# Kernel optimization log

Hardware: AMD Instinct MI355X
Metric: run time of the kernel (lower is better)

Reference implementation:

```python
import jax, jax.numpy as jnp
import numpy as np

N1, E1 = 102400, 300000
N2, E2 = 10240, 40960
N3, E3 = 1024, 4096
G = 64
D = 256   # node_dim == hidden_dim (forced by where(M==0, x, M))
B = 64    # bond_dim
DEPTHS = (3, 3, 4)


def _make_edges(rng, n_nodes, n_edges):
    # build mirrored directed edges so every edge has an exact reverse
    half = n_edges // 2
    u = rng.integers(0, n_nodes, half)
    v = rng.integers(0, n_nodes, half)
    src = np.concatenate([u, v])
    dst = np.concatenate([v, u])
    rev = np.concatenate([np.arange(half, n_edges), np.arange(0, half)])
    return np.stack([src, dst]).astype(np.int64), rev.astype(np.int64)


def _linear_params(key, fan_in, fan_out):
    k1, k2 = jax.random.split(key)
    s = 1.0 / np.sqrt(fan_in)
    W = jax.random.uniform(k1, (fan_in, fan_out), jnp.float32, -s, s)
    b = jax.random.uniform(k2, (fan_out,), jnp.float32, -s, s)
    return W, b


def setup_inputs() -> dict:
    rng = np.random.default_rng(0)
    key = jax.random.key(0)
    ks = jax.random.split(key, 16)

    ei1, rev1 = _make_edges(rng, N1, E1)
    ei2, rev2 = _make_edges(rng, N2, E2)
    ei3, rev3 = _make_edges(rng, N3, E3)

    inp = {
        "x": jax.random.normal(ks[0], (N1, D), jnp.float32),
        "edge_attr1": jax.random.normal(ks[1], (E1, B), jnp.float32),
        "edge_attr2": jax.random.normal(ks[2], (E2, B), jnp.float32),
        "edge_attr3": jax.random.normal(ks[3], (E3, B), jnp.float32),
        "edge_index1": jnp.asarray(ei1), "rev_edge_index1": jnp.asarray(rev1),
        "edge_index2": jnp.asarray(ei2), "rev_edge_index2": jnp.asarray(rev2),
        "edge_index3": jnp.asarray(ei3), "rev_edge_index3": jnp.asarray(rev3),
        "batch1_2": jnp.asarray(np.repeat(np.arange(N2), N1 // N2)),
        "batch2": jnp.asarray(np.repeat(np.arange(N3), N2 // N3)),
        "batch3": jnp.asarray(np.repeat(np.arange(G), N3 // G)),
    }
    kidx = 4
    for lvl in (1, 2, 3):
        Wi, bi = _linear_params(ks[kidx], D + B, D); kidx += 1
        Wh, bh = _linear_params(ks[kidx], D, D); kidx += 1
        Wo, bo = _linear_params(ks[kidx], D + D, D); kidx += 1
        inp[f"Wi{lvl}"], inp[f"bi{lvl}"] = Wi, bi
        inp[f"Wh{lvl}"], inp[f"bh{lvl}"] = Wh, bh
        inp[f"Wo{lvl}"], inp[f"bo{lvl}"] = Wo, bo
    return inp


def _bmp(x, src, dst, rev, ea, Wi, bi, Wh, bh, Wo, bo, depth):
    # BondMessagePassing.forward (dropout is identity in eval)
    n = x.shape[0]
    H0 = jax.nn.relu(jnp.concatenate([x[src], ea], axis=1) @ Wi + bi)  # [E, D]
    H = H0
    for _ in range(depth - 1):
        agg = jax.ops.segment_sum(H, dst, num_segments=n)              # [N, D]
        M = agg[src] - H[rev]
        H = jax.nn.relu(H0 + M @ Wh + bh)
    M = jax.ops.segment_sum(H, dst, num_segments=n)
    M = jnp.where(jnp.sum(M, axis=1, keepdims=True) == 0, x, M)
    return jax.nn.relu(jnp.concatenate([x, M], axis=1) @ Wo + bo)


def _mean_pool(h, seg, n):
    s = jax.ops.segment_sum(h, seg, num_segments=n)
    c = jax.ops.segment_sum(jnp.ones((h.shape[0], 1), h.dtype), seg, num_segments=n)
    return s / jnp.maximum(c, 1.0)


def reference(x, edge_attr1, edge_attr2, edge_attr3,
              edge_index1, rev_edge_index1, edge_index2, rev_edge_index2,
              edge_index3, rev_edge_index3, batch1_2, batch2, batch3,
              Wi1, bi1, Wh1, bh1, Wo1, bo1,
              Wi2, bi2, Wh2, bh2, Wo2, bo2,
              Wi3, bi3, Wh3, bh3, Wo3, bo3):
    h1 = _bmp(x, edge_index1[0], edge_index1[1], rev_edge_index1, edge_attr1,
              Wi1, bi1, Wh1, bh1, Wo1, bo1, DEPTHS[0])
    x2 = _mean_pool(h1, batch1_2, N2)
    h2 = _bmp(x2, edge_index2[0], edge_index2[1], rev_edge_index2, edge_attr2,
              Wi2, bi2, Wh2, bh2, Wo2, bo2, DEPTHS[1])
    x3 = _mean_pool(h2, batch2, N3)
    h3 = _bmp(x3, edge_index3[0], edge_index3[1], rev_edge_index3, edge_attr3,
              Wi3, bi3, Wh3, bh3, Wo3, bo3, DEPTHS[2])
    out = _mean_pool(h3, batch3, G)  # [G, D] subgraph3_pooled
    return out
```

## Files before the change

kernel.cpp:

```cpp
#include <hip/hip_runtime.h>
#include <stdint.h>

typedef __bf16 bf16;
typedef __bf16 bf16x4 __attribute__((ext_vector_type(4)));
typedef __bf16 bf16x8 __attribute__((ext_vector_type(8)));
typedef float  f32x4  __attribute__((ext_vector_type(4)));

__device__ __forceinline__ int clampi(int v, int n) { return (v < 0 || v >= n) ? 0 : v; }

__device__ __forceinline__ void gload16(const void* g, void* l) {
  __builtin_amdgcn_global_load_lds((const __attribute__((address_space(1))) void*)g,
                                   (__attribute__((address_space(3))) void*)l, 16, 0, 0);
}

__global__ void wtcvt_kernel(const float* __restrict__ W, bf16* __restrict__ Wt, int K) {
  int idx = blockIdx.x * 256 + threadIdx.x;
  if (idx >= K * 256) return;
  int k = idx >> 8, n = idx & 255;
  Wt[(size_t)n * K + k] = (bf16)W[idx];
}

__global__ void hist_kernel(const int* __restrict__ dst, int E, int* __restrict__ cnt, int N) {
  int e = blockIdx.x * 256 + threadIdx.x;
  if (e < E) atomicAdd(&cnt[clampi(dst[e], N)], 1);
}

__global__ void scan_block_kernel(const int* __restrict__ cnt, int N,
                                  int* __restrict__ incl, int* __restrict__ bsums) {
  __shared__ int sd[256];
  int t = threadIdx.x, bid = blockIdx.x;
  int base = bid * 1024 + t * 4;
  int v0 = (base + 0 < N) ? cnt[base + 0] : 0;
  int v1 = (base + 1 < N) ? cnt[base + 1] : 0;
  int v2 = (base + 2 < N) ? cnt[base + 2] : 0;
  int v3 = (base + 3 < N) ? cnt[base + 3] : 0;
  int s1 = v0 + v1, s2 = s1 + v2, s3 = s2 + v3;
  sd[t] = s3;
  __syncthreads();
  for (int off = 1; off < 256; off <<= 1) {
    int x = 0;
    if (t >= off) x = sd[t - off];
    __syncthreads();
    sd[t] += x;
    __syncthreads();
  }
  int excl = sd[t] - s3;
  if (base + 0 < N) incl[base + 0] = excl + v0;
  if (base + 1 < N) incl[base + 1] = excl + s1;
  if (base + 2 < N) incl[base + 2] = excl + s2;
  if (base + 3 < N) incl[base + 3] = excl + s3;
  if (t == 255) bsums[bid] = sd[255];
}

__global__ void scan_sums_kernel(const int* __restrict__ bsums, int nb, int* __restrict__ bexcl) {
  __shared__ int sd[256];
  int t = threadIdx.x;
  int v = (t < nb) ? bsums[t] : 0;
  sd[t] = v;
  __syncthreads();
  for (int off = 1; off < 256; off <<= 1) {
    int x = 0;
    if (t >= off) x = sd[t - off];
    __syncthreads();
    sd[t] += x;
    __syncthreads();
  }
  if (t < nb) bexcl[t] = sd[t] - v;
}

__global__ void scan_add_kernel(const int* __restrict__ incl, const int* __restrict__ bexcl,
                                int N, int* __restrict__ offs) {
  int i = blockIdx.x * 256 + threadIdx.x;
  if (i < N) offs[i + 1] = incl[i] + bexcl[i >> 10];
  if (i == 0) offs[0] = 0;
}

__global__ void scatter_kernel(const int* __restrict__ dst, int E, const int* __restrict__ offs,
                               int* __restrict__ cursor, int* __restrict__ elist, int N) {
  int e = blockIdx.x * 256 + threadIdx.x;
  if (e < E) {
    int d = clampi(dst[e], N);
    int p = atomicAdd(&cursor[d], 1);
    elist[offs[d] + p] = e;
  }
}

template <int WHERE, int XF32>
__global__ void segsum_kernel(const bf16* __restrict__ H, const int* __restrict__ elist,
                              const int* __restrict__ offs, const float* __restrict__ xf,
                              const bf16* __restrict__ xb, bf16* __restrict__ out, int N) {
  int lane = threadIdx.x & 63;
  int node = blockIdx.x * 4 + (threadIdx.x >> 6);
  if (node >= N) return;
  int beg = offs[node], end = offs[node + 1];
  float a0 = 0.f, a1 = 0.f, a2 = 0.f, a3 = 0.f;
  for (int p = beg; p < end; ++p) {
    int e = elist[p];
    bf16x4 v = ((const bf16x4*)(H + (size_t)e * 256))[lane];
    a0 += (float)v[0]; a1 += (float)v[1]; a2 += (float)v[2]; a3 += (float)v[3];
  }
  if (WHERE) {
    float s = a0 + a1 + a2 + a3;
    for (int off = 1; off < 64; off <<= 1) s += __shfl_xor(s, off);
    if (s == 0.f) {
      bf16x4 o;
      if (XF32) {
        float4 xv = ((const float4*)(xf))[(size_t)node * 64 + lane];
        o[0] = (bf16)xv.x; o[1] = (bf16)xv.y; o[2] = (bf16)xv.z; o[3] = (bf16)xv.w;
      } else {
        o = ((const bf16x4*)(xb + (size_t)node * 256))[lane];
      }
      ((bf16x4*)(out + (size_t)node * 256))[lane] = o;
      return;
    }
  }
  bf16x4 o = {(bf16)a0, (bf16)a1, (bf16)a2, (bf16)a3};
  ((bf16x4*)(out + (size_t)node * 256))[lane] = o;
}

template <int OUTF32>
__global__ void pool_kernel(const bf16* __restrict__ h, bf16* __restrict__ outb,
                            float* __restrict__ outf, int Nout, int cnt) {
  int lane = threadIdx.x & 63;
  int node = blockIdx.x * 4 + (threadIdx.x >> 6);
  if (node >= Nout) return;
  float a0 = 0.f, a1 = 0.f, a2 = 0.f, a3 = 0.f;
  size_t base = (size_t)node * cnt;
  for (int p = 0; p < cnt; ++p) {
    bf16x4 v = ((const bf16x4*)(h + (base + p) * 256))[lane];
    a0 += (float)v[0]; a1 += (float)v[1]; a2 += (float)v[2]; a3 += (float)v[3];
  }
  float c = (float)cnt;
  a0 /= c; a1 /= c; a2 /= c; a3 /= c;
  if (OUTF32) {
    float4 o = {a0, a1, a2, a3};
    ((float4*)(outf + (size_t)node * 256))[lane] = o;
  } else {
    bf16x4 o = {(bf16)a0, (bf16)a1, (bf16)a2, (bf16)a3};
    ((bf16x4*)(outb + (size_t)node * 256))[lane] = o;
  }
}

template <int MODE, int XF32>
__global__ __launch_bounds__(512, 4) void gemm_kernel(
    const float* __restrict__ A1f, const bf16* __restrict__ A1b,
    const float* __restrict__ A2f, const bf16* __restrict__ A2b,
    const bf16* __restrict__ Wt, const float* __restrict__ bias, const bf16* H0,
    const int* __restrict__ srcIdx, const int* __restrict__ revIdx,
    bf16* out, int Mrows, int K, int Nsrc) {
  __shared__ __align__(16) bf16 As[128 * 64];
  __shared__ __align__(16) bf16 Bs[256 * 64];
  int tid = threadIdx.x;
  int lane = tid & 63;
  int wave = tid >> 6;
  int wm = wave >> 2, wn = wave & 3;
  int m0 = blockIdx.x * 128;

  int rowA[2], uA[2];
  int base1[2], base2[2];
#pragma unroll
  for (int r = 0; r < 2; ++r) {
    int unit = r * 512 + tid;
    rowA[r] = unit >> 3;
    uA[r] = unit & 7;
    int rr = m0 + rowA[r];
    if (rr >= Mrows) rr = Mrows - 1;
    if (MODE == 0) {
      base1[r] = clampi(srcIdx[rr], Nsrc) * 256;
      base2[r] = rr * 64;
    } else if (MODE == 1) {
      base1[r] = clampi(srcIdx[rr], Nsrc) * 256;
      base2[r] = clampi(revIdx[rr], Mrows) * 256;
    } else {
      base1[r] = rr * 256;
      base2[r] = rr * 256;
    }
  }

  f32x4 acc[4][4];
#pragma unroll
  for (int i = 0; i < 4; ++i)
#pragma unroll
    for (int j = 0; j < 4; ++j) acc[i][j] = (f32x4){0.f, 0.f, 0.f, 0.f};

  float4 pf[2][2];

  auto loadA = [&](int kc) {
    int k0 = kc * 64;
#pragma unroll
    for (int r = 0; r < 2; ++r) {
      int u8 = uA[r] * 8;
      if (MODE == 0) {
        if (k0 < 256) {
          if (XF32) {
            const float* g = A1f + (size_t)(base1[r] + k0 + u8);
            pf[r][0] = *(const float4*)g;
            pf[r][1] = *(const float4*)(g + 4);
          } else {
            pf[r][0] = *(const float4*)(A1b + (size_t)(base1[r] + k0 + u8));
          }
        } else {
          const float* g = A2f + (size_t)(base2[r] + u8);
          pf[r][0] = *(const float4*)g;
          pf[r][1] = *(const float4*)(g + 4);
        }
      } else if (MODE == 1) {
        pf[r][0] = *(const float4*)(A1b + (size_t)(base1[r] + k0 + u8));
        pf[r][1] = *(const float4*)(A2b + (size_t)(base2[r] + k0 + u8));
      } else {
        if (k0 < 256) {
          if (XF32) {
            const float* g = A1f + (size_t)(base1[r] + k0 + u8);
            pf[r][0] = *(const float4*)g;
            pf[r][1] = *(const float4*)(g + 4);
          } else {
            pf[r][0] = *(const float4*)(A1b + (size_t)(base1[r] + k0 + u8));
          }
        } else {
          pf[r][0] = *(const float4*)(A2b + (size_t)(base2[r] + (k0 - 256) + u8));
        }
      }
    }
  };

  auto writeA = [&](int kc) {
    int k0 = kc * 64;
#pragma unroll
    for (int r = 0; r < 2; ++r) {
      int row = rowA[r], us = uA[r] ^ (row & 7);
      bf16x8 v;
      bool cvt32;
      if (MODE == 0) cvt32 = XF32 || (k0 >= 256);
      else if (MODE == 2) cvt32 = XF32 && (k0 < 256);
      else cvt32 = false;
      if (MODE == 1) {
        bf16x8 va = *(bf16x8*)(&pf[r][0]);
        bf16x8 vh = *(bf16x8*)(&pf[r][1]);
#pragma unroll
        for (int j = 0; j < 8; ++j) v[j] = (bf16)((float)va[j] - (float)vh[j]);
      } else if (cvt32) {
        const float* f = (const float*)&pf[r][0];
#pragma unroll
        for (int j = 0; j < 8; ++j) v[j] = (bf16)f[j];
      } else {
        v = *(bf16x8*)(&pf[r][0]);
      }
      *(bf16x8*)(&As[(size_t)(row * 8 + us) * 8]) = v;
    }
  };

  auto loadB = [&](int kc) {
    int k0 = kc * 64;
#pragma unroll
    for (int r = 0; r < 4; ++r) {
      int unit = r * 512 + tid;
      int row = unit >> 3, us = (unit & 7) ^ (row & 7);
      const bf16* g = Wt + (size_t)row * K + k0 + us * 8;
      bf16* l = &Bs[(size_t)(r * 512 + wave * 64) * 8];
      gload16(g, l);
    }
  };

  int nk = K / 64;
  loadA(0);
  for (int kc = 0; kc < nk; ++kc) {
    __syncthreads();
    writeA(kc);
    loadB(kc);
    __syncthreads();
    if (kc + 1 < nk) loadA(kc + 1);
#pragma unroll
    for (int s = 0; s < 2; ++s) {
      int kq = s * 4 + (lane >> 4);
      bf16x8 af[4], bfr[4];
#pragma unroll
      for (int i = 0; i < 4; ++i) {
        int arow = wm * 64 + i * 16 + (lane & 15);
        af[i] = *(const bf16x8*)(&As[(size_t)arow * 64 + (size_t)(kq ^ (arow & 7)) * 8]);
      }
#pragma unroll
      for (int j = 0; j < 4; ++j) {
        int brow = wn * 64 + j * 16 + (lane & 15);
        bfr[j] = *(const bf16x8*)(&Bs[(size_t)brow * 64 + (size_t)(kq ^ (brow & 7)) * 8]);
      }
#pragma unroll
      for (int i = 0; i < 4; ++i)
#pragma unroll
        for (int j = 0; j < 4; ++j)
          acc[i][j] = __builtin_amdgcn_mfma_f32_16x16x32_bf16(af[i], bfr[j], acc[i][j], 0, 0, 0);
    }
  }
#pragma unroll
  for (int i = 0; i < 4; ++i) {
    int rbase = m0 + wm * 64 + i * 16 + ((lane >> 4) << 2);
#pragma unroll
    for (int j = 0; j < 4; ++j) {
      int col = wn * 64 + j * 16 + (lane & 15);
      float bcol = bias[col];
#pragma unroll
      for (int r = 0; r < 4; ++r) {
        int row = rbase + r;
        if (row < Mrows) {
          float v = acc[i][j][r] + bcol;
          if (MODE == 1) v += (float)H0[(size_t)row * 256 + col];
          v = fmaxf(v, 0.f);
          out[(size_t)row * 256 + col] = (bf16)v;
        }
      }
    }
  }
}

template <int XF32>
static void run_level(const float* xf, const bf16* xb, const float* ea,
                      const int* src, const int* dst, const int* rev, int E, int N, int depth,
                      const bf16* WiT, const float* bi_, const bf16* WhT, const float* bh_,
                      const bf16* WoT, const float* bo_,
                      bf16* C, bf16* Dd, bf16* Ee, bf16* agg, bf16* h,
                      int* cnt, int* incl, int* offs, int* cursr, int* bsums, int* bexcl,
                      int* elist, hipStream_t stream) {
  hipMemsetAsync(cnt, 0, (size_t)N * 4, stream);
  hist_kernel<<<(E + 255) / 256, 256, 0, stream>>>(dst, E, cnt, N);
  int nb = (N + 1023) / 1024;
  scan_block_kernel<<<nb, 256, 0, stream>>>(cnt, N, incl, bsums);
  scan_sums_kernel<<<1, 256, 0, stream>>>(bsums, nb, bexcl);
  scan_add_kernel<<<(N + 255) / 256, 256, 0, stream>>>(incl, bexcl, N, offs);
  hipMemsetAsync(cursr, 0, (size_t)N * 4, stream);
  scatter_kernel<<<(E + 255) / 256, 256, 0, stream>>>(dst, E, offs, cursr, elist, N);

  dim3 ge((E + 127) / 128);
  gemm_kernel<0, XF32><<<ge, 512, 0, stream>>>(xf, xb, ea, nullptr, WiT, bi_, nullptr, src,
                                               nullptr, C, E, 320, N);
  bf16* Hcur = C;
  for (int it = 0; it < depth - 1; ++it) {
    segsum_kernel<0, 0><<<(N + 3) / 4, 256, 0, stream>>>(Hcur, elist, offs, nullptr, nullptr,
                                                         agg, N);
    bf16* Hn = (it == depth - 2) ? C : ((it & 1) ? Ee : Dd);
    gemm_kernel<1, 0><<<ge, 512, 0, stream>>>(nullptr, agg, nullptr, Hcur, WhT, bh_, C, src,
                                              rev, Hn, E, 256, N);
    Hcur = Hn;
  }
  segsum_kernel<1, XF32><<<(N + 3) / 4, 256, 0, stream>>>(Hcur, elist, offs, xf, xb, agg, N);
  dim3 gn((N + 127) / 128);
  gemm_kernel<2, XF32><<<gn, 512, 0, stream>>>(xf, xb, nullptr, agg, WoT, bo_, nullptr, nullptr,
                                               nullptr, h, N, 512, N);
}

extern "C" void kernel_launch(void* const* d_in, const int* in_sizes, int n_in,
                              void* d_out, int out_size, void* d_ws, size_t ws_size,
                              hipStream_t stream) {
  constexpr int N1 = 102400, E1 = 300000;
  constexpr int N2 = 10240, E2 = 40960;
  constexpr int N3 = 1024, E3 = 4096;
  constexpr int G = 64;
  constexpr int KI = 320, KH = 256, KO = 512;

  const float* x   = (const float*)d_in[0];
  const float* ea1 = (const float*)d_in[1];
  const float* ea2 = (const float*)d_in[2];
  const float* ea3 = (const float*)d_in[3];
  const int* ei1 = (const int*)d_in[4];
  const int* rv1 = (const int*)d_in[5];
  const int* ei2 = (const int*)d_in[6];
  const int* rv2 = (const int*)d_in[7];
  const int* ei3 = (const int*)d_in[8];
  const int* rv3 = (const int*)d_in[9];
  const float *Wi[3], *bi[3], *Wh[3], *bh[3], *Wo[3], *bo[3];
  for (int l = 0; l < 3; ++l) {
    Wi[l] = (const float*)d_in[13 + 6 * l + 0];
    bi[l] = (const float*)d_in[13 + 6 * l + 1];
    Wh[l] = (const float*)d_in[13 + 6 * l + 2];
    bh[l] = (const float*)d_in[13 + 6 * l + 3];
    Wo[l] = (const float*)d_in[13 + 6 * l + 4];
    bo[l] = (const float*)d_in[13 + 6 * l + 5];
  }
  float* outp = (float*)d_out;
  char* ws = (char*)d_ws;

  size_t off = 0;
  auto alloc = [&](size_t b) { size_t o = off; off += (b + 255) & ~(size_t)255; return o; };
  size_t o_wit[3], o_wht[3], o_wot[3];
  for (int l = 0; l < 3; ++l) {
    o_wit[l] = alloc((size_t)256 * KI * 2);
    o_wht[l] = alloc((size_t)256 * KH * 2);
    o_wot[l] = alloc((size_t)256 * KO * 2);
  }
  size_t o_C   = alloc((size_t)E1 * 256 * 2);
  size_t o_D   = alloc((size_t)E1 * 256 * 2);
  size_t o_E3b = alloc((size_t)E3 * 256 * 2);
  size_t o_agg = alloc((size_t)N1 * 256 * 2);
  size_t o_x2  = alloc((size_t)N2 * 256 * 2);
  size_t o_h2  = alloc((size_t)N2 * 256 * 2);
  size_t o_x3  = alloc((size_t)N3 * 256 * 2);
  size_t o_h3  = alloc((size_t)N3 * 256 * 2);
  size_t o_cnt = alloc((size_t)N1 * 4);
  size_t o_inc = alloc((size_t)N1 * 4);
  size_t o_off = alloc((size_t)(N1 + 1) * 4);
  size_t o_cur = alloc((size_t)N1 * 4);
  size_t o_bs  = alloc(1024 * 4);
  size_t o_bx  = alloc(1024 * 4);
  size_t o_el  = alloc((size_t)E1 * 4);

  if (ws_size < off) {
    hipMemsetAsync(d_out, 0, (size_t)out_size * 4, stream);
    return;
  }

  int* cnt   = (int*)(ws + o_cnt);
  int* incl  = (int*)(ws + o_inc);
  int* offs  = (int*)(ws + o_off);
  int* cursr = (int*)(ws + o_cur);
  int* bsums = (int*)(ws + o_bs);
  int* bexcl = (int*)(ws + o_bx);
  int* elist = (int*)(ws + o_el);
  bf16* C    = (bf16*)(ws + o_C);
  bf16* Dd   = (bf16*)(ws + o_D);
  bf16* E3b  = (bf16*)(ws + o_E3b);
  bf16* agg  = (bf16*)(ws + o_agg);
  bf16* x2b  = (bf16*)(ws + o_x2);
  bf16* h2b  = (bf16*)(ws + o_h2);
  bf16* x3b  = (bf16*)(ws + o_x3);
  bf16* h3b  = (bf16*)(ws + o_h3);

  for (int l = 0; l < 3; ++l) {
    wtcvt_kernel<<<(KI * 256 + 255) / 256, 256, 0, stream>>>(Wi[l], (bf16*)(ws + o_wit[l]), KI);
    wtcvt_kernel<<<(KH * 256 + 255) / 256, 256, 0, stream>>>(Wh[l], (bf16*)(ws + o_wht[l]), KH);
    wtcvt_kernel<<<(KO * 256 + 255) / 256, 256, 0, stream>>>(Wo[l], (bf16*)(ws + o_wot[l]), KO);
  }

  run_level<1>(x, nullptr, ea1, ei1, ei1 + E1, rv1, E1, N1, 3,
               (bf16*)(ws + o_wit[0]), bi[0], (bf16*)(ws + o_wht[0]), bh[0],
               (bf16*)(ws + o_wot[0]), bo[0], C, Dd, Dd, agg, C,
               cnt, incl, offs, cursr, bsums, bexcl, elist, stream);
  pool_kernel<0><<<(N2 + 3) / 4, 256, 0, stream>>>(C, x2b, nullptr, N2, N1 / N2);

  run_level<0>(nullptr, x2b, ea2, ei2, ei2 + E2, rv2, E2, N2, 3,
               (bf16*)(ws + o_wit[1]), bi[1], (bf16*)(ws + o_wht[1]), bh[1],
               (bf16*)(ws + o_wot[1]), bo[1], C, Dd, Dd, agg, h2b,
               cnt, incl, offs, cursr, bsums, bexcl, elist, stream);
  pool_kernel<0><<<(N3 + 3) / 4, 256, 0, stream>>>(h2b, x3b, nullptr, N3, N2 / N3);

  run_level<0>(nullptr, x3b, ea3, ei3, ei3 + E3, rv3, E3, N3, 4,
               (bf16*)(ws + o_wit[2]), bi[2], (bf16*)(ws + o_wht[2]), bh[2],
               (bf16*)(ws + o_wot[2]), bo[2], C, Dd, E3b, agg, h3b,
               cnt, incl, offs, cursr, bsums, bexcl, elist, stream);
  pool_kernel<1><<<(G + 3) / 4, 256, 0, stream>>>(h3b, nullptr, outp, G, N3 / G);
}
```

Measured before the change: 1.290 ms.

## Triple-buffer GEMM k-loop with compile-time unroll and pre-convert x to bf16

Rewrites the GEMM main loop as a fully unrolled, compile-time pipeline with three LDS buffers for A and B. Each k-step waits with a partial vmcnt barrier so B tiles and A register prefetches run two to three stages ahead of the MFMA work, replacing the two full __syncthreads per step. Launch bounds drop to 2 blocks per CU to make room for the larger LDS and register footprint. It also adds a kernel that converts the fp32 node features x to bf16 once, when workspace allows, so the level-1 gather reads half the bytes. The cost is lower occupancy and an extra conversion pass over x.

```diff
diff --git a/kernel.cpp b/kernel.cpp
--- a/kernel.cpp
+++ b/kernel.cpp
@@ -1,5 +1,6 @@
 #include <hip/hip_runtime.h>
 #include <stdint.h>
+#include <utility>
 
 typedef __bf16 bf16;
 typedef __bf16 bf16x4 __attribute__((ext_vector_type(4)));
@@ -11,6 +12,27 @@
 __device__ __forceinline__ void gload16(const void* g, void* l) {
   __builtin_amdgcn_global_load_lds((const __attribute__((address_space(1))) void*)g,
                                    (__attribute__((address_space(3))) void*)l, 16, 0, 0);
+}
+
+template <class F, int... I>
+__device__ __forceinline__ void unrolled(F&& f, std::integer_sequence<int, I...>) {
+  (f(std::integral_constant<int, I>{}), ...);
+}
+
+template <int N>
+__device__ __forceinline__ void wait_barrier() {
+  asm volatile("s_waitcnt vmcnt(%0) lgkmcnt(0)" ::"n"(N) : "memory");
+  __builtin_amdgcn_s_barrier();
+}
+
+__global__ void cvt_kernel(const float* __restrict__ in, bf16* __restrict__ out, int n8) {
+  int i = blockIdx.x * 256 + threadIdx.x;
+  if (i >= n8) return;
+  float4 a = ((const float4*)in)[i * 2];
+  float4 b = ((const float4*)in)[i * 2 + 1];
+  bf16x8 o = {(bf16)a.x, (bf16)a.y, (bf16)a.z, (bf16)a.w,
+              (bf16)b.x, (bf16)b.y, (bf16)b.z, (bf16)b.w};
+  ((bf16x8*)out)[i] = o;
 }
 
 __global__ void wtcvt_kernel(const float* __restrict__ W, bf16* __restrict__ Wt, int K) {
@@ -141,23 +163,37 @@
   }
 }
 
+template <int MODE, int XF32, int NK>
+constexpr int aCntF(int j) {
+  if (j < 0 || j >= NK) return 0;
+  if (MODE == 1) return 4;
+  if (MODE == 0) return (j == NK - 1) ? 4 : (XF32 ? 4 : 2);
+  return (XF32 && j < 4) ? 4 : 2;
+}
+template <int MODE, int XF32, int NK>
+constexpr int keepF(int kc) {
+  int b = (kc + 1 < NK) ? 4 : 0;
+  return b + aCntF<MODE, XF32, NK>(kc + 1) + aCntF<MODE, XF32, NK>(kc + 2);
+}
+
 template <int MODE, int XF32>
-__global__ __launch_bounds__(512, 4) void gemm_kernel(
+__global__ __launch_bounds__(512, 2) void gemm_kernel(
     const float* __restrict__ A1f, const bf16* __restrict__ A1b,
     const float* __restrict__ A2f, const bf16* __restrict__ A2b,
     const bf16* __restrict__ Wt, const float* __restrict__ bias, const bf16* H0,
     const int* __restrict__ srcIdx, const int* __restrict__ revIdx,
-    bf16* out, int Mrows, int K, int Nsrc) {
-  __shared__ __align__(16) bf16 As[128 * 64];
-  __shared__ __align__(16) bf16 Bs[256 * 64];
-  int tid = threadIdx.x;
-  int lane = tid & 63;
-  int wave = tid >> 6;
-  int wm = wave >> 2, wn = wave & 3;
-  int m0 = blockIdx.x * 128;
-
-  int rowA[2], uA[2];
-  int base1[2], base2[2];
+    bf16* out, int Mrows, int Nsrc) {
+  constexpr int KK = MODE == 0 ? 320 : (MODE == 1 ? 256 : 512);
+  constexpr int NK = KK / 64;
+  __shared__ __align__(16) bf16 As[3][128 * 64];
+  __shared__ __align__(16) bf16 Bs[3][256 * 64];
+  const int tid = threadIdx.x;
+  const int lane = tid & 63;
+  const int wave = tid >> 6;
+  const int wm = wave >> 2, wn = wave & 3;
+  const int m0 = blockIdx.x * 128;
+
+  int rowA[2], uA[2], base1[2], base2[2];
 #pragma unroll
   for (int r = 0; r < 2; ++r) {
     int unit = r * 512 + tid;
@@ -183,10 +219,22 @@
 #pragma unroll
     for (int j = 0; j < 4; ++j) acc[i][j] = (f32x4){0.f, 0.f, 0.f, 0.f};
 
-  float4 pf[2][2];
-
-  auto loadA = [&](int kc) {
-    int k0 = kc * 64;
+  float4 pf[3][2][2];
+
+  auto issueB = [&](auto KC_) {
+    constexpr int KC = decltype(KC_)::value;
+    constexpr int BUF = KC % 3;
+#pragma unroll
+    for (int r = 0; r < 4; ++r) {
+      int unit = r * 512 + tid;
+      int row = unit >> 3, us = (unit & 7) ^ (row & 7);
+      gload16(Wt + (size_t)row * KK + KC * 64 + us * 8, &Bs[BUF][(r * 512 + wave * 64) * 8]);
+    }
+  };
+  auto loadA = [&](auto KC_) {
+    constexpr int KC = decltype(KC_)::value;
+    constexpr int S = KC % 3;
+    constexpr int k0 = KC * 64;
 #pragma unroll
     for (int r = 0; r < 2; ++r) {
       int u8 = uA[r] * 8;
@@ -194,81 +242,64 @@
         if (k0 < 256) {
           if (XF32) {
             const float* g = A1f + (size_t)(base1[r] + k0 + u8);
-            pf[r][0] = *(const float4*)g;
-            pf[r][1] = *(const float4*)(g + 4);
+            pf[S][r][0] = *(const float4*)g;
+            pf[S][r][1] = *(const float4*)(g + 4);
           } else {
-            pf[r][0] = *(const float4*)(A1b + (size_t)(base1[r] + k0 + u8));
+            pf[S][r][0] = *(const float4*)(A1b + (size_t)(base1[r] + k0 + u8));
           }
         } else {
           const float* g = A2f + (size_t)(base2[r] + u8);
-          pf[r][0] = *(const float4*)g;
-          pf[r][1] = *(const float4*)(g + 4);
+          pf[S][r][0] = *(const float4*)g;
+          pf[S][r][1] = *(const float4*)(g + 4);
         }
       } else if (MODE == 1) {
-        pf[r][0] = *(const float4*)(A1b + (size_t)(base1[r] + k0 + u8));
-        pf[r][1] = *(const float4*)(A2b + (size_t)(base2[r] + k0 + u8));
+        pf[S][r][0] = *(const float4*)(A1b + (size_t)(base1[r] + k0 + u8));
+        pf[S][r][1] = *(const float4*)(A2b + (size_t)(base2[r] + k0 + u8));
       } else {
         if (k0 < 256) {
           if (XF32) {
             const float* g = A1f + (size_t)(base1[r] + k0 + u8);
-            pf[r][0] = *(const float4*)g;
-            pf[r][1] = *(const float4*)(g + 4);
+            pf[S][r][0] = *(const float4*)g;
+            pf[S][r][1] = *(const float4*)(g + 4);
           } else {
-            pf[r][0] = *(const float4*)(A1b + (size_t)(base1[r] + k0 + u8));
+            pf[S][r][0] = *(const float4*)(A1b + (size_t)(base1[r] + k0 + u8));
           }
         } else {
-          pf[r][0] = *(const float4*)(A2b + (size_t)(base2[r] + (k0 - 256) + u8));
+          pf[S][r][0] = *(const float4*)(A2b + (size_t)(base2[r] + (k0 - 256) + u8));
         }
       }
     }
   };
-
-  auto writeA = [&](int kc) {
-    int k0 = kc * 64;
+  auto writeA = [&](auto KC_) {
+    constexpr int KC = decltype(KC_)::value;
+    constexpr int S = KC % 3;
+    constexpr int k0 = KC * 64;
 #pragma unroll
     for (int r = 0; r < 2; ++r) {
       int row = rowA[r], us = uA[r] ^ (row & 7);
       bf16x8 v;
-      bool cvt32;
-      if (MODE == 0) cvt32 = XF32 || (k0 >= 256);
-      else if (MODE == 2) cvt32 = XF32 && (k0 < 256);
-      else cvt32 = false;
+      constexpr bool cvt32 = (MODE == 0) ? (XF32 || k0 >= 256)
+                           : (MODE == 2) ? (XF32 && k0 < 256) : false;
       if (MODE == 1) {
-        bf16x8 va = *(bf16x8*)(&pf[r][0]);
-        bf16x8 vh = *(bf16x8*)(&pf[r][1]);
+        bf16x8 va = *(bf16x8*)&pf[S][r][0];
+        bf16x8 vh = *(bf16x8*)&pf[S][r][1];
 #pragma unroll
         for (int j = 0; j < 8; ++j) v[j] = (bf16)((float)va[j] - (float)vh[j]);
       } else if (cvt32) {
-        const float* f = (const float*)&pf[r][0];
+        const float* f = (const float*)&pf[S][r][0];
 #pragma unroll
         for (int j = 0; j < 8; ++j) v[j] = (bf16)f[j];
       } else {
-        v = *(bf16x8*)(&pf[r][0]);
+        v = *(bf16x8*)&pf[S][r][0];
       }
-      *(bf16x8*)(&As[(size_t)(row * 8 + us) * 8]) = v;
+      *(bf16x8*)(&As[S][((size_t)row * 8 + us) * 8]) = v;
     }
   };
-
-  auto loadB = [&](int kc) {
-    int k0 = kc * 64;
-#pragma unroll
-    for (int r = 0; r < 4; ++r) {
-      int unit = r * 512 + tid;
-      int row = unit >> 3, us = (unit & 7) ^ (row & 7);
-      const bf16* g = Wt + (size_t)row * K + k0 + us * 8;
-      bf16* l = &Bs[(size_t)(r * 512 + wave * 64) * 8];
-      gload16(g, l);
-    }
-  };
-
-  int nk = K / 64;
-  loadA(0);
-  for (int kc = 0; kc < nk; ++kc) {
-    __syncthreads();
-    writeA(kc);
-    loadB(kc);
-    __syncthreads();
-    if (kc + 1 < nk) loadA(kc + 1);
+  auto compute = [&](auto KC_) {
+    constexpr int KC = decltype(KC_)::value;
+    constexpr int BUF = KC % 3;
+    const bf16* Asb = As[BUF];
+    const bf16* Bsb = Bs[BUF];
 #pragma unroll
     for (int s = 0; s < 2; ++s) {
       int kq = s * 4 + (lane >> 4);
@@ -276,12 +307,12 @@
 #pragma unroll
       for (int i = 0; i < 4; ++i) {
         int arow = wm * 64 + i * 16 + (lane & 15);
-        af[i] = *(const bf16x8*)(&As[(size_t)arow * 64 + (size_t)(kq ^ (arow & 7)) * 8]);
+        af[i] = *(const bf16x8*)(&Asb[(size_t)arow * 64 + (size_t)(kq ^ (arow & 7)) * 8]);
       }
 #pragma unroll
       for (int j = 0; j < 4; ++j) {
         int brow = wn * 64 + j * 16 + (lane & 15);
-        bfr[j] = *(const bf16x8*)(&Bs[(size_t)brow * 64 + (size_t)(kq ^ (brow & 7)) * 8]);
+        bfr[j] = *(const bf16x8*)(&Bsb[(size_t)brow * 64 + (size_t)(kq ^ (brow & 7)) * 8]);
       }
 #pragma unroll
       for (int i = 0; i < 4; ++i)
@@ -289,7 +320,24 @@
         for (int j = 0; j < 4; ++j)
           acc[i][j] = __builtin_amdgcn_mfma_f32_16x16x32_bf16(af[i], bfr[j], acc[i][j], 0, 0, 0);
     }
-  }
+  };
+
+  issueB(std::integral_constant<int, 0>{});
+  loadA(std::integral_constant<int, 0>{});
+  issueB(std::integral_constant<int, 1>{});
+  loadA(std::integral_constant<int, 1>{});
+  writeA(std::integral_constant<int, 0>{});
+  loadA(std::integral_constant<int, 2>{});
+
+  unrolled([&](auto kc_) {
+    constexpr int kc = decltype(kc_)::value;
+    wait_barrier<keepF<MODE, XF32, NK>(kc)>();
+    if constexpr (kc + 2 < NK) issueB(std::integral_constant<int, kc + 2>{});
+    if constexpr (kc + 3 < NK) loadA(std::integral_constant<int, kc + 3>{});
+    compute(kc_);
+    if constexpr (kc + 1 < NK) writeA(std::integral_constant<int, kc + 1>{});
+  }, std::make_integer_sequence<int, NK>{});
+
 #pragma unroll
   for (int i = 0; i < 4; ++i) {
     int rbase = m0 + wm * 64 + i * 16 + ((lane >> 4) << 2);
@@ -330,20 +378,20 @@
 
   dim3 ge((E + 127) / 128);
   gemm_kernel<0, XF32><<<ge, 512, 0, stream>>>(xf, xb, ea, nullptr, WiT, bi_, nullptr, src,
-                                               nullptr, C, E, 320, N);
+                                               nullptr, C, E, N);
   bf16* Hcur = C;
   for (int it = 0; it < depth - 1; ++it) {
     segsum_kernel<0, 0><<<(N + 3) / 4, 256, 0, stream>>>(Hcur, elist, offs, nullptr, nullptr,
                                                          agg, N);
     bf16* Hn = (it == depth - 2) ? C : ((it & 1) ? Ee : Dd);
     gemm_kernel<1, 0><<<ge, 512, 0, stream>>>(nullptr, agg, nullptr, Hcur, WhT, bh_, C, src,
-                                              rev, Hn, E, 256, N);
+                                              rev, Hn, E, N);
     Hcur = Hn;
   }
   segsum_kernel<1, XF32><<<(N + 3) / 4, 256, 0, stream>>>(Hcur, elist, offs, xf, xb, agg, N);
   dim3 gn((N + 127) / 128);
   gemm_kernel<2, XF32><<<gn, 512, 0, stream>>>(xf, xb, nullptr, agg, WoT, bo_, nullptr, nullptr,
-                                               nullptr, h, N, 512, N);
+                                               nullptr, h, N, N);
 }
 
 extern "C" void kernel_launch(void* const* d_in, const int* in_sizes, int n_in,
@@ -400,11 +448,15 @@
   size_t o_bs  = alloc(1024 * 4);
   size_t o_bx  = alloc(1024 * 4);
   size_t o_el  = alloc((size_t)E1 * 4);
-
-  if (ws_size < off) {
+  size_t need_base = off;
+  size_t o_xb = alloc((size_t)N1 * 256 * 2);
+  size_t need_ext = off;
+
+  if (ws_size < need_base) {
     hipMemsetAsync(d_out, 0, (size_t)out_size * 4, stream);
     return;
   }
+  const bool use_xb = (ws_size >= need_ext);
 
   int* cnt   = (int*)(ws + o_cnt);
   int* incl  = (int*)(ws + o_inc);
@@ -421,6 +473,7 @@
   bf16* h2b  = (bf16*)(ws + o_h2);
   bf16* x3b  = (bf16*)(ws + o_x3);
   bf16* h3b  = (bf16*)(ws + o_h3);
+  bf16* xbp  = (bf16*)(ws + o_xb);
 
   for (int l = 0; l < 3; ++l) {
     wtcvt_kernel<<<(KI * 256 + 255) / 256, 256, 0, stream>>>(Wi[l], (bf16*)(ws + o_wit[l]), KI);
@@ -428,10 +481,18 @@
     wtcvt_kernel<<<(KO * 256 + 255) / 256, 256, 0, stream>>>(Wo[l], (bf16*)(ws + o_wot[l]), KO);
   }
 
-  run_level<1>(x, nullptr, ea1, ei1, ei1 + E1, rv1, E1, N1, 3,
-               (bf16*)(ws + o_wit[0]), bi[0], (bf16*)(ws + o_wht[0]), bh[0],
-               (bf16*)(ws + o_wot[0]), bo[0], C, Dd, Dd, agg, C,
-               cnt, incl, offs, cursr, bsums, bexcl, elist, stream);
+  if (use_xb) {
+    cvt_kernel<<<(N1 * 256 / 8 + 255) / 256, 256, 0, stream>>>(x, xbp, N1 * 256 / 8);
+    run_level<0>(nullptr, xbp, ea1, ei1, ei1 + E1, rv1, E1, N1, 3,
+                 (bf16*)(ws + o_wit[0]), bi[0], (bf16*)(ws + o_wht[0]), bh[0],
+                 (bf16*)(ws + o_wot[0]), bo[0], C, Dd, Dd, agg, C,
+                 cnt, incl, offs, cursr, bsums, bexcl, elist, stream);
+  } else {
+    run_level<1>(x, nullptr, ea1, ei1, ei1 + E1, rv1, E1, N1, 3,
+                 (bf16*)(ws + o_wit[0]), bi[0], (bf16*)(ws + o_wht[0]), bh[0],
+                 (bf16*)(ws + o_wot[0]), bo[0], C, Dd, Dd, agg, C,
+                 cnt, incl, offs, cursr, bsums, bexcl, elist, stream);
+  }
   pool_kernel<0><<<(N2 + 3) / 4, 256, 0, stream>>>(C, x2b, nullptr, N2, N1 / N2);
 
   run_level<0>(nullptr, x2b, ea2, ei2, ei2 + E2, rv2, E2, N2, 3,
```

New measurement: 1.334 ms. +3.4%, slower.
